# Kernel optimization log

Hardware: AMD Instinct MI355X
Metric: run time of the kernel (lower is better)

## Reference

```python
import jax, jax.numpy as jnp
import numpy as np
from jax import lax

T = 64      # timesteps == number of stacked LSTM layers (per source)
B = 128     # lstm_batchsize (hardcoded)
H = 64      # BasicLSTMCell(64)


def _cell(x_in, c, h, W, b):
    # TF BasicLSTMCell, forget_bias=0.0, gate order: i, j, f, o
    z = jnp.concatenate([x_in, h], axis=-1) @ W + b          # [B, 4H]
    i, j, f, o = jnp.split(z, 4, axis=-1)
    c2 = c * jax.nn.sigmoid(f) + jax.nn.sigmoid(i) * jnp.tanh(j)
    h2 = jnp.tanh(c2) * jax.nn.sigmoid(o)
    return c2, h2


def setup_inputs() -> dict:
    key = jax.random.key(0)
    ks = jax.random.split(key, 8)
    s = 0.1
    x = jax.random.normal(ks[0], (B, T, 1), dtype=jnp.float32)
    labels = jax.random.normal(ks[1], (B, T, 1), dtype=jnp.float32)
    # layer 0: input dim 1; layers 1..T-1: input dim H
    W0 = jax.random.normal(ks[2], (1 + H, 4 * H), dtype=jnp.float32) * s
    b0 = jnp.zeros((4 * H,), dtype=jnp.float32)
    Wl = jax.random.normal(ks[3], (T - 1, H + H, 4 * H), dtype=jnp.float32) * s
    bl = jnp.zeros((T - 1, 4 * H), dtype=jnp.float32)
    # time_distributed fully_connected(1, relu): separate weights per timestep
    Wd = jax.random.normal(ks[4], (T, H, 1), dtype=jnp.float32) * s
    bd = jnp.zeros((T, 1), dtype=jnp.float32)
    return {"x": x, "labels": labels, "W0": W0, "b0": b0,
            "Wl": Wl, "bl": bl, "Wd": Wd, "bd": bd}


def reference(x, labels, W0, b0, Wl, bl, Wd, bd):
    def step(carry, x_t):
        cs, hs = carry                      # each [T, B, H]
        c0, h0 = _cell(x_t, cs[0], hs[0], W0, b0)

        def layer_step(h_in, lp):
            c, h_prev, W, b = lp
            c2, h2 = _cell(h_in, c, h_prev, W, b)
            return h2, (c2, h2)

        h_top, (cs_r, hs_r) = lax.scan(layer_step, h0, (cs[1:], hs[1:], Wl, bl))
        new_cs = jnp.concatenate([c0[None], cs_r], axis=0)
        new_hs = jnp.concatenate([h0[None], hs_r], axis=0)
        return (new_cs, new_hs), h_top

    init = (jnp.zeros((T, B, H), x.dtype), jnp.zeros((T, B, H), x.dtype))
    xs = jnp.transpose(x, (1, 0, 2))        # [T, B, 1]
    _, outs = lax.scan(step, init, xs)      # outs: [T, B, H]
    outs = jnp.transpose(outs, (1, 0, 2))   # [B, T, H]

    # per-timestep dense + relu
    pred = jax.nn.relu(jnp.einsum('bth,tho->bto', outs, Wd) + bd[None])  # [B, T, 1]
    loss = jnp.mean(jnp.square(labels - pred))
    return pred, loss
```

## Files before the change

kernel.cpp:

```cpp
#include <hip/hip_runtime.h>
#include <hip/hip_bf16.h>
#include <hip/hip_fp8.h>

#define TT 64
#define LL 64
#define BB 128
#define HH 64
#define GG 4
#define NG 16
#define SL 8
#define RR 16
#define SB (TT + GG - 1)

typedef short v8s __attribute__((ext_vector_type(8)));
typedef float v4f __attribute__((ext_vector_type(4)));


__device__ __forceinline__ float sigm(float z)   {
    return __builtin_amdgcn_rcpf(1.f + __expf(-z));
}
__device__ __forceinline__ float tanh_f(float z) {
    return fmaf(-2.f, __builtin_amdgcn_rcpf(1.f + __expf(2.f * z)), 1.f);
}

__device__ __forceinline__ void poll4(const unsigned long long* base,
                                      unsigned long long& v0, unsigned long long& v1,
                                      unsigned long long& v2, unsigned long long& v3) {
    asm volatile(
        "global_load_dwordx2 %0, %4, off sc0 sc1\n\t"
        "global_load_dwordx2 %1, %4, off offset:8 sc0 sc1\n\t"
        "global_load_dwordx2 %2, %4, off offset:64 sc0 sc1\n\t"
        "global_load_dwordx2 %3, %4, off offset:72 sc0 sc1\n\t"
        "s_waitcnt vmcnt(0)"
        : "=v"(v0), "=v"(v1), "=v"(v2), "=v"(v3)
        : "v"(base)
        : "memory");
}
__device__ __forceinline__ void gstore64(unsigned long long* p, unsigned long long v) {
    asm volatile("global_store_dwordx2 %0, %1, off sc0 sc1"
                 :: "v"(p), "v"(v) : "memory");
}
__device__ __forceinline__ int fload(const int* p) {
    int v;
    asm volatile("global_load_dword %0, %1, off sc0 sc1\n\ts_waitcnt vmcnt(0)"
                 : "=v"(v) : "v"(p) : "memory");
    return v;
}
__device__ __forceinline__ void fstore(int* p, int v) {
    asm volatile("global_store_dword %0, %1, off sc0 sc1"
                 :: "v"(p), "v"(v) : "memory");
}
__device__ __forceinline__ unsigned short f2bf(float f) {
    unsigned u = __float_as_uint(f);
    return (unsigned short)((u + 0x8000u) >> 16);
}

__global__ __launch_bounds__(512, 2) void lstm_pipeline(
    const float* __restrict__ x,
    const float* __restrict__ W0,
    const float* __restrict__ b0,
    const float* __restrict__ Wl,
    const float* __restrict__ bl,
    int* __restrict__ prog,
    unsigned long long* __restrict__ hglob,
    float* __restrict__ htop)
{
    const int g   = blockIdx.x >> 3;
    const int s   = blockIdx.x & 7;
    const int tid = threadIdx.x;
    const int wv  = tid >> 6;
    const int k   = wv >> 1;
    const int nh  = wv & 1;
    const int ln  = tid & 63;
    const int lr  = ln & 15;
    const int qd  = ln >> 4;
    const int l   = GG * g + k;

    __shared__ unsigned short hL[GG][2][RR * 72];
    __shared__ float xbuf[RR * 65];

    if (blockIdx.x == 0 && tid < 2) fstore(&prog[300 + tid], 0);

    for (int i = tid; i < GG * 2 * RR * 72; i += 512)
        ((unsigned short*)hL)[i] = 0;
    if (g == 0) {
        for (int i = tid; i < RR * 64; i += 512)
            xbuf[(i >> 6) * 65 + (i & 63)] =
                x[(size_t)(s * RR + (i >> 6)) * TT + (i & 63)];
    }

    v8s bfr[32];
#pragma unroll
    for (int f = 0; f < 32; ++f) {
        const int kf = f & 3, tn = f >> 2;
        const int ga = tn & 3, ut = tn >> 2;
        const int gc = ga * 64 + nh * 32 + ut * 16 + lr;
        v8s tmp;
#pragma unroll
        for (int j = 0; j < 8; ++j) {
            const int kk = kf * 32 + qd * 8 + j;
            float v;
            if (l > 0)        v = Wl[((size_t)(l - 1) * 128 + kk) * 256 + gc];
            else if (kk == 0) v = W0[gc];
            else if (kk < 64) v = 0.f;
            else              v = W0[(size_t)(kk - 63) * 256 + gc];
            tmp[j] = (short)f2bf(v);
        }
        bfr[f] = tmp;
    }

    const float* bs = l ? (bl + (l - 1) * 256) : b0;
    float bias[8];
#pragma unroll
    for (int i = 0; i < 8; ++i) {
        const int ut = i >> 2, ga = i & 3;
        bias[i] = bs[ga * 64 + nh * 32 + ut * 16 + lr];
    }

    float cst[8];
#pragma unroll
    for (int i = 0; i < 8; ++i) cst[i] = 0.f;

    __syncthreads();

    for (int sb = 0; sb < SB; ++sb) {
        const int t = sb - k;
        const bool active = (t >= 0) && (t < TT);
        const int rd = (sb - 1) & 1, wr = sb & 1;

        if (active) {
            const int row = lr * 72;
            v8s a2 = *(const v8s*)&hL[k][rd][row + qd * 8];
            v8s a3 = *(const v8s*)&hL[k][rd][row + 32 + qd * 8];
            v8s a0, a1;
            if (k > 0) {
                a0 = *(const v8s*)&hL[k - 1][rd][row + qd * 8];
                a1 = *(const v8s*)&hL[k - 1][rd][row + 32 + qd * 8];
            } else if (g > 0) {
                const unsigned long long* rp =
                    hglob + ((((size_t)(t & 15) * NG + (g - 1)) * SL + s) * RR + lr) * 16
                          + qd * 2;
                unsigned int bw0, bw1, bw2, bw3;
                for (;;) {
                    unsigned long long v0, v1, v2, v3;
                    poll4(rp, v0, v1, v2, v3);
                    unsigned int ok =
                        (unsigned int)((unsigned int)(v0 >> 32) == (unsigned int)t) &
                        (unsigned int)((unsigned int)(v1 >> 32) == (unsigned int)t) &
                        (unsigned int)((unsigned int)(v2 >> 32) == (unsigned int)t) &
                        (unsigned int)((unsigned int)(v3 >> 32) == (unsigned int)t);
                    if (ok) {
                        bw0 = (unsigned int)v0; bw1 = (unsigned int)v1;
                        bw2 = (unsigned int)v2; bw3 = (unsigned int)v3;
                        break;
                    }
                }
                if (nh == 0 && ln == 0) fstore(&prog[s * NG + g], t + 1);
                unsigned int ws4[4] = {bw0, bw1, bw2, bw3};
#pragma unroll
                for (int wi = 0; wi < 2; ++wi)
#pragma unroll
                    for (int bi = 0; bi < 4; ++bi) {
                        __hip_fp8_e4m3 f8;
                        f8.__x = (ws4[wi] >> (8 * bi)) & 0xff;
                        a0[wi * 4 + bi] = (short)f2bf((float)f8);
                        f8.__x = (ws4[2 + wi] >> (8 * bi)) & 0xff;
                        a1[wi * 4 + bi] = (short)f2bf((float)f8);
                    }
            } else {
                a0 = (v8s){0, 0, 0, 0, 0, 0, 0, 0};
                a1 = (v8s){0, 0, 0, 0, 0, 0, 0, 0};
                if (qd == 0) a0[0] = (short)f2bf(xbuf[lr * 65 + t]);
            }

            v4f acc[8];
#pragma unroll
            for (int i = 0; i < 8; ++i) acc[i] = (v4f){0.f, 0.f, 0.f, 0.f};
#pragma unroll
            for (int tn = 0; tn < 8; ++tn) {
                v4f c = acc[tn];
                c = __builtin_amdgcn_mfma_f32_16x16x32_bf16(a2, bfr[tn * 4 + 2], c, 0, 0, 0);
                c = __builtin_amdgcn_mfma_f32_16x16x32_bf16(a3, bfr[tn * 4 + 3], c, 0, 0, 0);
                c = __builtin_amdgcn_mfma_f32_16x16x32_bf16(a0, bfr[tn * 4 + 0], c, 0, 0, 0);
                c = __builtin_amdgcn_mfma_f32_16x16x32_bf16(a1, bfr[tn * 4 + 1], c, 0, 0, 0);
                acc[tn] = c;
            }

            if (k == 3 && g < NG - 1 && t >= 14)
                while (fload(&prog[s * NG + (g + 1)]) < t - 14) {}

            unsigned long long* dst =
                hglob + ((((size_t)(t & 15) * NG + g) * SL + s) * RR) * 16;
#pragma unroll
            for (int ut = 0; ut < 2; ++ut) {
                const int u = nh * 32 + ut * 16 + lr;
#pragma unroll
                for (int r = 0; r < 4; ++r) {
                    float zi = acc[ut * 4 + 0][r] + bias[ut * 4 + 0];
                    float zj = acc[ut * 4 + 1][r] + bias[ut * 4 + 1];
                    float zf = acc[ut * 4 + 2][r] + bias[ut * 4 + 2];
                    float zo = acc[ut * 4 + 3][r] + bias[ut * 4 + 3];
                    float c2 = cst[ut * 4 + r] * sigm(zf) + sigm(zi) * tanh_f(zj);
                    cst[ut * 4 + r] = c2;
                    float h2 = tanh_f(c2) * sigm(zo);
                    const int b = qd * 4 + r;
                    hL[k][wr][b * 72 + u] = f2bf(h2);
                    if (k == 3) {
                        if (g < NG - 1) {
                            __hip_fp8_e4m3 f8(h2);
                            unsigned int pk = ((unsigned int)f8.__x) << (8 * (lr & 3));
                            pk |= __shfl_xor(pk, 1);
                            pk |= __shfl_xor(pk, 2);
                            if ((lr & 3) == 0)
                                gstore64(dst + (size_t)b * 16 + nh * 8 + ut * 4 + (lr >> 2),
                                         (unsigned long long)pk |
                                         ((unsigned long long)(unsigned int)t << 32));
                        } else {
                            htop[((size_t)t * HH + u) * BB + s * RR + b] = h2;
                        }
                    }
                }
            }
        }
        __syncthreads();
    }
}

__global__ __launch_bounds__(128, 1) void epilogue(
    const float* __restrict__ htop, const float* __restrict__ Wd,
    const float* __restrict__ bd, const float* __restrict__ labels,
    float* __restrict__ out, int* __restrict__ prog)
{
    int t = blockIdx.x, b = threadIdx.x;
    float s = 0.f;
#pragma unroll 4
    for (int h = 0; h < HH; ++h)
        s = fmaf(htop[(size_t)t * HH * BB + h * BB + b], Wd[t * HH + h], s);
    s += bd[t];
    s = fmaxf(s, 0.f);
    out[b * TT + t] = s;
    float d = labels[b * TT + t] - s;
    float e = d * d;
#pragma unroll
    for (int off = 32; off > 0; off >>= 1) e += __shfl_down(e, off, 64);
    __shared__ float ws2[2];
    if ((b & 63) == 0) ws2[b >> 6] = e;
    __syncthreads();
    if (b == 0) {
        float* loss = (float*)&prog[300];
        atomicAdd(loss, ws2[0] + ws2[1]);
        __builtin_amdgcn_s_waitcnt(0);
        int done = __hip_atomic_fetch_add(&prog[301], 1, __ATOMIC_ACQ_REL,
                                          __HIP_MEMORY_SCOPE_AGENT);
        if (done == 63) {
            float tot = __hip_atomic_load(loss, __ATOMIC_RELAXED,
                                          __HIP_MEMORY_SCOPE_AGENT);
            out[BB * TT] = tot * (1.f / (BB * TT));
        }
    }
}

extern "C" void kernel_launch(void* const* d_in, const int* in_sizes, int n_in,
                              void* d_out, int out_size, void* d_ws, size_t ws_size,
                              hipStream_t stream) {
    const float* x      = (const float*)d_in[0];
    const float* labels = (const float*)d_in[1];
    const float* W0     = (const float*)d_in[2];
    const float* b0     = (const float*)d_in[3];
    const float* Wl     = (const float*)d_in[4];
    const float* bl     = (const float*)d_in[5];
    const float* Wd     = (const float*)d_in[6];
    const float* bd     = (const float*)d_in[7];
    float* out = (float*)d_out;

    char* base = (char*)d_ws;
    int*                prog  = (int*)base;
    unsigned long long* hglob = (unsigned long long*)(base + 16384);
    float*              htop  = (float*)(base + 16384 + 4194304);

    lstm_pipeline<<<NG * SL, 512, 0, stream>>>(x, W0, b0, Wl, bl, prog, hglob, htop);
    epilogue<<<64, 128, 0, stream>>>(htop, Wd, bd, labels, out, prog);
}
```

Before: 516.1 us.

## Dual-path inter-block handoff with fast cached copy, batched backpressure, lighter barrier

Each cross-block hidden-state message is now written twice: once with default cache policy into a new fast buffer and once with system-coherent sc0 sc1 stores into the original buffer. Consumers poll both copies and take whichever already carries the current timestep tag, hoping the fast path delivers sooner. Backpressure polling on the downstream block's progress counter now runs only every 8th step with a tighter lag bound, which cuts how often it polls. __syncthreads is replaced by an lgkmcnt wait plus s_barrier, so the barrier no longer waits on outstanding global memory ops. The cost is doubled stores, doubled poll loads, and dependence on the fast non-coherent copy becoming visible across CUs.

```diff
diff --git a/kernel.cpp b/kernel.cpp
--- a/kernel.cpp
+++ b/kernel.cpp
@@ -23,22 +23,31 @@
     return fmaf(-2.f, __builtin_amdgcn_rcpf(1.f + __expf(2.f * z)), 1.f);
 }
 
-__device__ __forceinline__ void poll4(const unsigned long long* base,
-                                      unsigned long long& v0, unsigned long long& v1,
-                                      unsigned long long& v2, unsigned long long& v3) {
+__device__ __forceinline__ void poll8(const unsigned long long* fast,
+                                      const unsigned long long* ins,
+                                      unsigned long long* f, unsigned long long* i) {
     asm volatile(
-        "global_load_dwordx2 %0, %4, off sc0 sc1\n\t"
-        "global_load_dwordx2 %1, %4, off offset:8 sc0 sc1\n\t"
-        "global_load_dwordx2 %2, %4, off offset:64 sc0 sc1\n\t"
-        "global_load_dwordx2 %3, %4, off offset:72 sc0 sc1\n\t"
+        "global_load_dwordx2 %0, %8, off sc0\n\t"
+        "global_load_dwordx2 %1, %8, off offset:8 sc0\n\t"
+        "global_load_dwordx2 %2, %8, off offset:64 sc0\n\t"
+        "global_load_dwordx2 %3, %8, off offset:72 sc0\n\t"
+        "global_load_dwordx2 %4, %9, off sc0 sc1\n\t"
+        "global_load_dwordx2 %5, %9, off offset:8 sc0 sc1\n\t"
+        "global_load_dwordx2 %6, %9, off offset:64 sc0 sc1\n\t"
+        "global_load_dwordx2 %7, %9, off offset:72 sc0 sc1\n\t"
         "s_waitcnt vmcnt(0)"
-        : "=v"(v0), "=v"(v1), "=v"(v2), "=v"(v3)
-        : "v"(base)
+        : "=v"(f[0]), "=v"(f[1]), "=v"(f[2]), "=v"(f[3]),
+          "=v"(i[0]), "=v"(i[1]), "=v"(i[2]), "=v"(i[3])
+        : "v"(fast), "v"(ins)
         : "memory");
 }
-__device__ __forceinline__ void gstore64(unsigned long long* p, unsigned long long v) {
-    asm volatile("global_store_dwordx2 %0, %1, off sc0 sc1"
-                 :: "v"(p), "v"(v) : "memory");
+__device__ __forceinline__ void gstore64_dual(unsigned long long* pf,
+                                              unsigned long long* pi,
+                                              unsigned long long v) {
+    asm volatile(
+        "global_store_dwordx2 %0, %2, off\n\t"
+        "global_store_dwordx2 %1, %2, off sc0 sc1"
+        :: "v"(pf), "v"(pi), "v"(v) : "memory");
 }
 __device__ __forceinline__ int fload(const int* p) {
     int v;
@@ -49,6 +58,9 @@
 __device__ __forceinline__ void fstore(int* p, int v) {
     asm volatile("global_store_dword %0, %1, off sc0 sc1"
                  :: "v"(p), "v"(v) : "memory");
+}
+__device__ __forceinline__ void barrier_lds() {
+    asm volatile("s_waitcnt lgkmcnt(0)\n\ts_barrier" ::: "memory");
 }
 __device__ __forceinline__ unsigned short f2bf(float f) {
     unsigned u = __float_as_uint(f);
@@ -62,7 +74,8 @@
     const float* __restrict__ Wl,
     const float* __restrict__ bl,
     int* __restrict__ prog,
-    unsigned long long* __restrict__ hglob,
+    unsigned long long* __restrict__ hglobI,
+    unsigned long long* __restrict__ hglobF,
     float* __restrict__ htop)
 {
     const int g   = blockIdx.x >> 3;
@@ -137,21 +150,22 @@
                 a0 = *(const v8s*)&hL[k - 1][rd][row + qd * 8];
                 a1 = *(const v8s*)&hL[k - 1][rd][row + 32 + qd * 8];
             } else if (g > 0) {
-                const unsigned long long* rp =
-                    hglob + ((((size_t)(t & 15) * NG + (g - 1)) * SL + s) * RR + lr) * 16
-                          + qd * 2;
+                const size_t off =
+                    ((((size_t)(t & 15) * NG + (g - 1)) * SL + s) * RR + lr) * 16 + qd * 2;
                 unsigned int bw0, bw1, bw2, bw3;
                 for (;;) {
-                    unsigned long long v0, v1, v2, v3;
-                    poll4(rp, v0, v1, v2, v3);
-                    unsigned int ok =
-                        (unsigned int)((unsigned int)(v0 >> 32) == (unsigned int)t) &
-                        (unsigned int)((unsigned int)(v1 >> 32) == (unsigned int)t) &
-                        (unsigned int)((unsigned int)(v2 >> 32) == (unsigned int)t) &
-                        (unsigned int)((unsigned int)(v3 >> 32) == (unsigned int)t);
-                    if (ok) {
-                        bw0 = (unsigned int)v0; bw1 = (unsigned int)v1;
-                        bw2 = (unsigned int)v2; bw3 = (unsigned int)v3;
+                    unsigned long long f4[4], i4[4];
+                    poll8(hglobF + off, hglobI + off, f4, i4);
+                    unsigned int okF = 1, okI = 1;
+#pragma unroll
+                    for (int q2 = 0; q2 < 4; ++q2) {
+                        okF &= (unsigned int)((unsigned int)(f4[q2] >> 32) == (unsigned int)t);
+                        okI &= (unsigned int)((unsigned int)(i4[q2] >> 32) == (unsigned int)t);
+                    }
+                    if (okF | okI) {
+                        const unsigned long long* pick = okF ? f4 : i4;
+                        bw0 = (unsigned int)pick[0]; bw1 = (unsigned int)pick[1];
+                        bw2 = (unsigned int)pick[2]; bw3 = (unsigned int)pick[3];
                         break;
                     }
                 }
@@ -186,11 +200,10 @@
                 acc[tn] = c;
             }
 
-            if (k == 3 && g < NG - 1 && t >= 14)
-                while (fload(&prog[s * NG + (g + 1)]) < t - 14) {}
-
-            unsigned long long* dst =
-                hglob + ((((size_t)(t & 15) * NG + g) * SL + s) * RR) * 16;
+            if (k == 3 && g < NG - 1 && t >= 16 && (t & 7) == 0)
+                while (fload(&prog[s * NG + (g + 1)]) < t - 7) {}
+
+            const size_t dbase = (((size_t)(t & 15) * NG + g) * SL + s) * RR * 16;
 #pragma unroll
             for (int ut = 0; ut < 2; ++ut) {
                 const int u = nh * 32 + ut * 16 + lr;
@@ -211,10 +224,12 @@
                             unsigned int pk = ((unsigned int)f8.__x) << (8 * (lr & 3));
                             pk |= __shfl_xor(pk, 1);
                             pk |= __shfl_xor(pk, 2);
-                            if ((lr & 3) == 0)
-                                gstore64(dst + (size_t)b * 16 + nh * 8 + ut * 4 + (lr >> 2),
-                                         (unsigned long long)pk |
-                                         ((unsigned long long)(unsigned int)t << 32));
+                            if ((lr & 3) == 0) {
+                                const size_t o = dbase + (size_t)b * 16 + nh * 8 + ut * 4 + (lr >> 2);
+                                gstore64_dual(hglobF + o, hglobI + o,
+                                              (unsigned long long)pk |
+                                              ((unsigned long long)(unsigned int)t << 32));
+                            }
                         } else {
                             htop[((size_t)t * HH + u) * BB + s * RR + b] = h2;
                         }
@@ -222,7 +237,7 @@
                 }
             }
         }
-        __syncthreads();
+        barrier_lds();
     }
 }
 
@@ -274,10 +289,12 @@
     float* out = (float*)d_out;
 
     char* base = (char*)d_ws;
-    int*                prog  = (int*)base;
-    unsigned long long* hglob = (unsigned long long*)(base + 16384);
-    float*              htop  = (float*)(base + 16384 + 4194304);
-
-    lstm_pipeline<<<NG * SL, 512, 0, stream>>>(x, W0, b0, Wl, bl, prog, hglob, htop);
+    int*                prog   = (int*)base;
+    unsigned long long* hglobI = (unsigned long long*)(base + 16384);
+    unsigned long long* hglobF = (unsigned long long*)(base + 16384 + 4194304);
+    float*              htop   = (float*)(base + 16384 + 8388608);
+
+    lstm_pipeline<<<NG * SL, 512, 0, stream>>>(x, W0, b0, Wl, bl, prog,
+                                               hglobI, hglobF, htop);
     epilogue<<<64, 128, 0, stream>>>(htop, Wd, bd, labels, out, prog);
 }
```

Measured after the change: 487.8 us. 1.06x faster.
